# Performance work log

Measured on AMD Instinct MI355X. Metric: run time of the kernel, lower is better.

Reference implementation:

```python
import jax, jax.numpy as jnp
import numpy as np

N = 8192          # number of nodes
A = 3             # number of adjacency relations
D_IN = 256
D_OUT = 64


def setup_inputs() -> dict:
    key = jax.random.key(0)
    k1, k2, k3, k4 = jax.random.split(key, 4)
    inputs = jax.random.normal(k1, (N, D_IN), dtype=jnp.float32)
    # dense adjacency stack [A, N, N] (weighted graph)
    adj_set = jax.random.uniform(k2, (A, N, N), dtype=jnp.float32)
    att = jax.random.uniform(k3, (A,), dtype=jnp.float32)
    w = jax.random.normal(k4, (D_IN, D_OUT), dtype=jnp.float32) * (1.0 / np.sqrt(D_IN))
    b = jnp.zeros((D_OUT,), dtype=jnp.float32)
    return {"inputs": inputs, "adj_set": adj_set, "att": att, "w": w, "b": b}


def reference(inputs, adj_set, att, w, b):
    # dropout=False -> identity; note: self.relu is never applied in forward
    support = jnp.matmul(inputs, w) + b                      # [N, D_OUT]
    # outputs = sum_i att[i] * (adj_i @ support), fused as one einsum
    outputs = jnp.einsum("a,anm,md->nd", att, adj_set, support)
    return outputs
```

## Files before the change

kernel.cpp:

```cpp
#include <hip/hip_runtime.h>
#include <hip/hip_bf16.h>


#define NNODES 8192
#define DIN    256
#define DOUT   64
#define NA     3
#define KSTACK (NA * NNODES)
#define KQ     (KSTACK / 4)
#define BK     256
#define NCH    (KQ / BK)
#define NSTRIP (NNODES / 64)

typedef float f32x4 __attribute__((ext_vector_type(4)));
typedef short s16x8 __attribute__((ext_vector_type(8)));

__device__ __forceinline__ unsigned short f2bf(float f) {
    __hip_bfloat16 h = __float2bfloat16(f);
    return __builtin_bit_cast(unsigned short, h);
}

__device__ __forceinline__ s16x8 pack8(f32x4 a, f32x4 b) {
    s16x8 o;
    o[0] = (short)f2bf(a[0]); o[1] = (short)f2bf(a[1]);
    o[2] = (short)f2bf(a[2]); o[3] = (short)f2bf(a[3]);
    o[4] = (short)f2bf(b[0]); o[5] = (short)f2bf(b[1]);
    o[6] = (short)f2bf(b[2]); o[7] = (short)f2bf(b[3]);
    return o;
}

__device__ __forceinline__ void gload_lds16(const float* g, float* l) {
    __builtin_amdgcn_global_load_lds(
        (const __attribute__((address_space(1))) void*)g,
        (__attribute__((address_space(3))) void*)l, 16, 0, 2);
}

__global__ __launch_bounds__(256) void zero_out(float* __restrict__ out) {
    f32x4 z = {0.f, 0.f, 0.f, 0.f};
    ((f32x4*)out)[(blockIdx.x << 8) + threadIdx.x] = z;
}

__global__ __launch_bounds__(256) void prep_support(
    const float* __restrict__ x, const float* __restrict__ w,
    const float* __restrict__ bias, const float* __restrict__ att,
    unsigned short* __restrict__ Bp)
{
    const int t = threadIdx.x;
    const int d = t & 63;
    const int m = (blockIdx.x << 2) + (t >> 6);

    const float* xr = x + (size_t)m * DIN;
    float acc = bias[d];
#pragma unroll 4
    for (int k = 0; k < DIN; k += 4) {
        f32x4 xv = *(const f32x4*)(xr + k);
        acc += xv[0] * w[(k + 0) * DOUT + d];
        acc += xv[1] * w[(k + 1) * DOUT + d];
        acc += xv[2] * w[(k + 2) * DOUT + d];
        acc += xv[3] * w[(k + 3) * DOUT + d];
    }

    const int kt   = m >> 5;
    const int kl   = m & 31;
    const int lane = ((kl >> 3) << 4) | (d & 15);
    const int j    = kl & 7;
    const int nt   = d >> 4;

    const size_t base    = (size_t)(kt * 4 + nt) * 512 + lane * 8 + j;
    const size_t aStride = (size_t)(NNODES / 32) * 4 * 512;

    const float a0 = att[0], a1 = att[1], a2 = att[2];
    Bp[base]               = f2bf(a0 * acc);
    Bp[base + aStride]     = f2bf(a1 * acc);
    Bp[base + 2 * aStride] = f2bf(a2 * acc);
}

template <bool ATOMIC>
__global__ __launch_bounds__(256, 2) void graphconv_gemm(
    const float* __restrict__ adj, const unsigned short* __restrict__ Bp,
    float* __restrict__ dst)
{
    __shared__ float ldsf[16384];

    const int tid  = threadIdx.x;
    const int wv   = tid >> 6;
    const int lane = tid & 63;
    const int r    = lane & 15;
    const int g    = lane >> 4;
    const int r7   = r & 7;
    const int q     = blockIdx.x & 3;
    const int strip = blockIdx.x >> 2;
    const int row0  = strip * 64 + wv * 16;

    float* wbuf = &ldsf[wv << 12];

    f32x4 acc0 = {0.f, 0.f, 0.f, 0.f};
    f32x4 acc1 = {0.f, 0.f, 0.f, 0.f};
    f32x4 acc2 = {0.f, 0.f, 0.f, 0.f};
    f32x4 acc3 = {0.f, 0.f, 0.f, 0.f};

    const int c0 = (wv * 6 + strip) % NCH;

    for (int i = 0; i < NCH; ++i) {
        int c = c0 + i; if (c >= NCH) c -= NCH;
        const int k0 = q * KQ + c * BK;
        const float* ab = adj + ((size_t)(k0 >> 13) << 26) + (k0 & 8191);

#pragma unroll
        for (int p = 0; p < 16; ++p) {
            const float* gp = ab + (size_t)(row0 + p) * NNODES
                                 + ((lane ^ (p & 7)) << 2);
            gload_lds16(gp, wbuf + (p << 8));
        }
        asm volatile("s_waitcnt vmcnt(0)" ::: "memory");
        __builtin_amdgcn_sched_barrier(0);

        const s16x8* bp = (const s16x8*)Bp + ((size_t)(k0 >> 5) << 8) + lane;
        const float* lrow = wbuf + (r << 8);
#pragma unroll
        for (int t = 0; t < 8; ++t) {
            f32x4 v0 = *(const f32x4*)(lrow + ((t * 8 + ((2 * g) ^ r7)) << 2));
            f32x4 v1 = *(const f32x4*)(lrow + ((t * 8 + ((2 * g + 1) ^ r7)) << 2));
            s16x8 af = pack8(v0, v1);
            s16x8 b0 = bp[0];
            s16x8 b1 = bp[64];
            s16x8 b2 = bp[128];
            s16x8 b3 = bp[192];
            acc0 = __builtin_amdgcn_mfma_f32_16x16x32_bf16(af, b0, acc0, 0, 0, 0);
            acc1 = __builtin_amdgcn_mfma_f32_16x16x32_bf16(af, b1, acc1, 0, 0, 0);
            acc2 = __builtin_amdgcn_mfma_f32_16x16x32_bf16(af, b2, acc2, 0, 0, 0);
            acc3 = __builtin_amdgcn_mfma_f32_16x16x32_bf16(af, b3, acc3, 0, 0, 0);
            bp += 256;
        }
    }

    if (ATOMIC) {
        float* op = dst + (size_t)row0 * DOUT;
#pragma unroll
        for (int j = 0; j < 4; ++j) {
            float* rp = op + (size_t)(4 * g + j) * DOUT + r;
            atomicAdd(rp,      acc0[j]);
            atomicAdd(rp + 16, acc1[j]);
            atomicAdd(rp + 32, acc2[j]);
            atomicAdd(rp + 48, acc3[j]);
        }
    } else {
        float* pp = dst + (size_t)q * (NNODES * DOUT) + (size_t)row0 * DOUT;
#pragma unroll
        for (int j = 0; j < 4; ++j) {
            float* rp = pp + (size_t)(4 * g + j) * DOUT + r;
            rp[0]  = acc0[j];
            rp[16] = acc1[j];
            rp[32] = acc2[j];
            rp[48] = acc3[j];
        }
    }
}

__global__ __launch_bounds__(256) void reduce_partials(
    const float* __restrict__ part, float* __restrict__ out)
{
    const int i = (blockIdx.x << 8) + threadIdx.x;
    const f32x4* p = (const f32x4*)part;
    f32x4 s = p[i] + p[i + 131072] + p[i + 262144] + p[i + 393216];
    ((f32x4*)out)[i] = s;
}

extern "C" void kernel_launch(void* const* d_in, const int* in_sizes, int n_in,
                              void* d_out, int out_size, void* d_ws, size_t ws_size,
                              hipStream_t stream) {
    const float* x   = (const float*)d_in[0];
    const float* adj = (const float*)d_in[1];
    const float* att = (const float*)d_in[2];
    const float* w   = (const float*)d_in[3];
    const float* b   = (const float*)d_in[4];
    float* out = (float*)d_out;

    unsigned short* Bp = (unsigned short*)d_ws;
    const size_t bpBytes   = (size_t)KSTACK * DOUT * 2;
    const size_t partOff   = (bpBytes + 255) & ~(size_t)255;
    const size_t partBytes = (size_t)4 * NNODES * DOUT * 4;
    const bool usePartials = ws_size >= partOff + partBytes;

    prep_support<<<NNODES / 4, 256, 0, stream>>>(x, w, b, att, Bp);

    if (usePartials) {
        float* part = (float*)((char*)d_ws + partOff);
        graphconv_gemm<false><<<NSTRIP * 4, 256, 0, stream>>>(adj, Bp, part);
        reduce_partials<<<NNODES * DOUT / 1024, 256, 0, stream>>>(part, out);
    } else {
        zero_out<<<NNODES * DOUT / 1024, 256, 0, stream>>>(out);
        graphconv_gemm<true><<<NSTRIP * 4, 256, 0, stream>>>(adj, Bp, out);
    }
}
```

Measured before the change: 185.2 us.

## Double-buffer adjacency tiles in LDS with halved K chunk and prefetched B fragments

The K chunk is halved and the per-wave LDS tile is split into two buffers, so the global-to-LDS loads for the next chunk are issued before the MFMAs on the current chunk. A partial vmcnt wait lets those loads overlap compute instead of stalling on a full drain every chunk. All B fragments for the chunk are loaded into registers up front. In exchange, register pressure rises (16 s16x8 B values) and the loop runs twice as many iterations. The vmcnt(8) count depends on the compiler's exact ordering of the memory instructions.

```diff
diff --git a/kernel.cpp b/kernel.cpp
--- a/kernel.cpp
+++ b/kernel.cpp
@@ -8,7 +8,7 @@
 #define NA     3
 #define KSTACK (NA * NNODES)
 #define KQ     (KSTACK / 4)
-#define BK     256
+#define BK     128
 #define NCH    (KQ / BK)
 #define NSTRIP (NNODES / 64)
 
@@ -80,7 +80,7 @@
     const float* __restrict__ adj, const unsigned short* __restrict__ Bp,
     float* __restrict__ dst)
 {
-    __shared__ float ldsf[16384];
+    __shared__ float ldsf[2][4][2048];
 
     const int tid  = threadIdx.x;
     const int wv   = tid >> 6;
@@ -92,45 +92,75 @@
     const int strip = blockIdx.x >> 2;
     const int row0  = strip * 64 + wv * 16;
 
-    float* wbuf = &ldsf[wv << 12];
+    const int prow = lane >> 5;
+    const int slot = lane & 31;
 
     f32x4 acc0 = {0.f, 0.f, 0.f, 0.f};
     f32x4 acc1 = {0.f, 0.f, 0.f, 0.f};
     f32x4 acc2 = {0.f, 0.f, 0.f, 0.f};
     f32x4 acc3 = {0.f, 0.f, 0.f, 0.f};
 
-    const int c0 = (wv * 6 + strip) % NCH;
+    const int c0 = (wv * 12 + strip) % NCH;
+
+    {
+        const int k0 = q * KQ + c0 * BK;
+        const float* ab = adj + ((size_t)(k0 >> 13) << 26) + (k0 & 8191);
+        float* wbuf = &ldsf[0][wv][0];
+#pragma unroll
+        for (int j = 0; j < 8; ++j) {
+            const int p = 2 * j + prow;
+            const float* gp = ab + (size_t)(row0 + p) * NNODES
+                                 + ((slot ^ (p & 7)) << 2);
+            gload_lds16(gp, wbuf + (j << 8));
+        }
+    }
 
     for (int i = 0; i < NCH; ++i) {
         int c = c0 + i; if (c >= NCH) c -= NCH;
-        const int k0 = q * KQ + c * BK;
-        const float* ab = adj + ((size_t)(k0 >> 13) << 26) + (k0 & 8191);
-
-#pragma unroll
-        for (int p = 0; p < 16; ++p) {
-            const float* gp = ab + (size_t)(row0 + p) * NNODES
-                                 + ((lane ^ (p & 7)) << 2);
-            gload_lds16(gp, wbuf + (p << 8));
-        }
-        asm volatile("s_waitcnt vmcnt(0)" ::: "memory");
+        const int k0  = q * KQ + c * BK;
+        const int cur = i & 1;
+
+        const s16x8* bp = (const s16x8*)Bp + ((size_t)(k0 >> 5) << 8) + lane;
+        s16x8 bq[16];
+#pragma unroll
+        for (int t = 0; t < 4; ++t)
+#pragma unroll
+            for (int n = 0; n < 4; ++n)
+                bq[t * 4 + n] = bp[t * 256 + n * 64];
+
         __builtin_amdgcn_sched_barrier(0);
 
-        const s16x8* bp = (const s16x8*)Bp + ((size_t)(k0 >> 5) << 8) + lane;
-        const float* lrow = wbuf + (r << 8);
-#pragma unroll
-        for (int t = 0; t < 8; ++t) {
-            f32x4 v0 = *(const f32x4*)(lrow + ((t * 8 + ((2 * g) ^ r7)) << 2));
-            f32x4 v1 = *(const f32x4*)(lrow + ((t * 8 + ((2 * g + 1) ^ r7)) << 2));
+        const bool more = (i + 1 < NCH);
+        if (more) {
+            int cn = c + 1; if (cn >= NCH) cn = 0;
+            const int kn = q * KQ + cn * BK;
+            const float* ab = adj + ((size_t)(kn >> 13) << 26) + (kn & 8191);
+            float* nbuf = &ldsf[cur ^ 1][wv][0];
+#pragma unroll
+            for (int j = 0; j < 8; ++j) {
+                const int p = 2 * j + prow;
+                const float* gp = ab + (size_t)(row0 + p) * NNODES
+                                     + ((slot ^ (p & 7)) << 2);
+                gload_lds16(gp, nbuf + (j << 8));
+            }
+            asm volatile("s_waitcnt vmcnt(8)" ::: "memory");
+        } else {
+            asm volatile("s_waitcnt vmcnt(0)" ::: "memory");
+        }
+        __builtin_amdgcn_sched_barrier(0);
+
+        const float* lrow = &ldsf[cur][wv][0] + (r << 7);
+#pragma unroll
+        for (int t = 0; t < 4; ++t) {
+            const int s0 = (t * 8 + 2 * g)     ^ r7;
+            const int s1 = (t * 8 + 2 * g + 1) ^ r7;
+            f32x4 v0 = *(const f32x4*)(lrow + (s0 << 2));
+            f32x4 v1 = *(const f32x4*)(lrow + (s1 << 2));
             s16x8 af = pack8(v0, v1);
-            s16x8 b0 = bp[0];
-            s16x8 b1 = bp[64];
-            s16x8 b2 = bp[128];
-            s16x8 b3 = bp[192];
-            acc0 = __builtin_amdgcn_mfma_f32_16x16x32_bf16(af, b0, acc0, 0, 0, 0);
-            acc1 = __builtin_amdgcn_mfma_f32_16x16x32_bf16(af, b1, acc1, 0, 0, 0);
-            acc2 = __builtin_amdgcn_mfma_f32_16x16x32_bf16(af, b2, acc2, 0, 0, 0);
-            acc3 = __builtin_amdgcn_mfma_f32_16x16x32_bf16(af, b3, acc3, 0, 0, 0);
-            bp += 256;
+            acc0 = __builtin_amdgcn_mfma_f32_16x16x32_bf16(af, bq[t*4+0], acc0, 0, 0, 0);
+            acc1 = __builtin_amdgcn_mfma_f32_16x16x32_bf16(af, bq[t*4+1], acc1, 0, 0, 0);
+            acc2 = __builtin_amdgcn_mfma_f32_16x16x32_bf16(af, bq[t*4+2], acc2, 0, 0, 0);
+            acc3 = __builtin_amdgcn_mfma_f32_16x16x32_bf16(af, bq[t*4+3], acc3, 0, 0, 0);
         }
     }
 
```

Result: slower. 194.4 us (+5.0%).
